# Kernel optimization log

Measured on AMD Instinct MI355X. Metric: run time of the kernel, lower is better.

The kernel has to match this reference:

```python
import jax, jax.numpy as jnp
import numpy as np


def setup_inputs() -> dict:
    key = jax.random.key(0)
    kx, ky = jax.random.split(key)
    x = jax.random.normal(kx, (4, 8192, 3), dtype=jnp.float32)
    y = jax.random.normal(ky, (4, 8192, 3), dtype=jnp.float32)
    return {"x": x, "y": y}


def _chamfer(x, y):
    # x: [B, N, D], y: [B, M, D]
    x2 = jnp.sum(x * x, axis=-1)                      # [B, N]
    y2 = jnp.sum(y * y, axis=-1)                      # [B, M]
    xy = jnp.einsum("bnd,bmd->bnm", x, y)             # [B, N, M]
    d2 = x2[:, :, None] + y2[:, None, :] - 2.0 * xy   # [B, N, M]
    d2 = jnp.maximum(d2, 0.0)
    cham_x = jnp.min(d2, axis=2).mean(axis=1)         # [B] min over M, mean over N
    cham_y = jnp.min(d2, axis=1).mean(axis=1)         # [B] min over N, mean over M
    return cham_x + cham_y                            # [B]


def reference(x, y):
    per_batch = _chamfer(x, y)
    return jnp.mean(per_batch)  # batch_reduction='mean'
```

## Files before the change

### kernel.cpp

```cpp
#include <hip/hip_runtime.h>


#define N_      8192
#define RPB     4096
#define NRECS   16384
#define NQ      65536
#define FLT_BIG 3.0e38f

typedef float v2f  __attribute__((ext_vector_type(2)));
typedef unsigned int v16u __attribute__((ext_vector_type(16)));

__global__ void zero_out_kernel(float* out) { *out = 0.0f; }

__global__ __launch_bounds__(256) void prep_kernel(
    const float* __restrict__ x, const float* __restrict__ y,
    float4* __restrict__ xrec, float4* __restrict__ yrec,
    unsigned int* __restrict__ pmin, float* __restrict__ out)
{
    int i = blockIdx.x * 256 + threadIdx.x;
    if (i == 0) *out = 0.0f;
    pmin[i]         = 0x7F800000u;
    pmin[i + 32768] = 0x7F800000u;
    int side = i >> 14;
    int r    = i & (NRECS - 1);
    const float* src = side ? y : x;
    float4*      dst = side ? yrec : xrec;
    const float* p = src + (size_t)r * 6;
    float p0x = p[0], p0y = p[1], p0z = p[2];
    float p1x = p[3], p1y = p[4], p1z = p[5];
    float w0 = fmaf(p0x, p0x, fmaf(p0y, p0y, p0z * p0z));
    float w1 = fmaf(p1x, p1x, fmaf(p1y, p1y, p1z * p1z));
    dst[2*r]   = make_float4(p0x, p1x, p0y, p1y);
    dst[2*r+1] = make_float4(p0z, p1z, w0, w1);
}


static __device__ __forceinline__ void s_load2(v16u& a, v16u& b, const unsigned int* p) {
    asm volatile("s_load_dwordx16 %0, %2, 0x0\n\t"
                 "s_load_dwordx16 %1, %2, 0x40"
                 : "=s"(a), "=s"(b) : "s"(p));
}
static __device__ __forceinline__ void s_wait(v16u& a, v16u& b) {
    asm volatile("s_waitcnt lgkmcnt(0)" : "+s"(a), "+s"(b));
}

static __device__ __forceinline__ void do_record(
    const unsigned int* d,
    const v2f* qx, const v2f* qy, const v2f* qz,
    float* acc)
{
    v2f pxs = (v2f){__uint_as_float(d[0]), __uint_as_float(d[1])};
    v2f pys = (v2f){__uint_as_float(d[2]), __uint_as_float(d[3])};
    v2f pzs = (v2f){__uint_as_float(d[4]), __uint_as_float(d[5])};
    v2f w2v = (v2f){__uint_as_float(d[6]), __uint_as_float(d[7])};
    #pragma unroll
    for (int j = 0; j < 4; ++j) {
        v2f td, ts;
        asm("v_pk_fma_f32 %0, %1, %2, %3"
            : "=v"(td) : "v"(qz[j]), "s"(pzs), "v"(w2v));
        asm("v_pk_fma_f32 %0, %1, %2, %3 op_sel:[0,1,1] op_sel_hi:[1,0,0]"
            : "=v"(ts) : "v"(qz[j]), "s"(pzs), "v"(w2v));
        asm("v_pk_fma_f32 %0, %1, %2, %0"
            : "+v"(td) : "v"(qy[j]), "s"(pys));
        asm("v_pk_fma_f32 %0, %1, %2, %0 op_sel:[0,1,0] op_sel_hi:[1,0,1]"
            : "+v"(ts) : "v"(qy[j]), "s"(pys));
        asm("v_pk_fma_f32 %0, %1, %2, %0"
            : "+v"(td) : "v"(qx[j]), "s"(pxs));
        asm("v_pk_fma_f32 %0, %1, %2, %0 op_sel:[0,1,0] op_sel_hi:[1,0,1]"
            : "+v"(ts) : "v"(qx[j]), "s"(pxs));
        asm("v_min3_f32 %0, %0, %1, %2" : "+v"(acc[2*j])   : "v"(td.x), "v"(ts.x));
        asm("v_min3_f32 %0, %0, %1, %2" : "+v"(acc[2*j+1]) : "v"(td.y), "v"(ts.y));
    }
}

__global__ __launch_bounds__(512, 4) void chamfer_kernel(
    const float* __restrict__ xraw, const float* __restrict__ yraw,
    const float4* __restrict__ xrec, const float4* __restrict__ yrec,
    unsigned int* __restrict__ pmin)
{
    __shared__ float red[8 * 512];

    const int tid  = threadIdx.x;
    const int lane = tid & 63;
    const int wave = __builtin_amdgcn_readfirstlane(tid >> 6);
    const int blk  = blockIdx.x;
    const int dir   = blk >> 8;
    const int batch = (blk >> 6) & 3;
    const int qg    = (blk >> 2) & 15;
    const int seg   = blk & 3;

    const float*  qraw = dir ? yraw : xraw;
    const float4* orec = dir ? xrec : yrec;

    const int qbase = batch * N_ + qg * 512;
    float f[24];
    {
        const float4* qv = (const float4*)(qraw + (size_t)qbase * 3) + lane * 6;
        #pragma unroll
        for (int k = 0; k < 6; ++k) {
            float4 t = qv[k];
            f[4*k] = t.x; f[4*k+1] = t.y; f[4*k+2] = t.z; f[4*k+3] = t.w;
        }
    }
    v2f qx[4], qy[4], qz[4];
    float acc[8];
    #pragma unroll
    for (int j = 0; j < 4; ++j) {
        qx[j] = (v2f){-2.0f * f[6*j+0], -2.0f * f[6*j+3]};
        qy[j] = (v2f){-2.0f * f[6*j+1], -2.0f * f[6*j+4]};
        qz[j] = (v2f){-2.0f * f[6*j+2], -2.0f * f[6*j+5]};
        acc[2*j] = FLT_BIG; acc[2*j+1] = FLT_BIG;
    }

    const unsigned int* sp = (const unsigned int*)
        (orec + (size_t)2 * (batch * RPB + seg * 1024 + wave * 128));
    v16u a0, a1, b0, b1;
    s_load2(a0, a1, sp);
    for (int g = 0; g < 32; g += 2) {
        s_wait(a0, a1);
        if (g + 1 < 32) s_load2(b0, b1, sp + (g + 1) * 32);
        {
            unsigned int da[16], db[16];
            #pragma unroll
            for (int t = 0; t < 16; ++t) { da[t] = a0[t]; db[t] = a1[t]; }
            do_record(da,     qx, qy, qz, acc);
            do_record(da + 8, qx, qy, qz, acc);
            do_record(db,     qx, qy, qz, acc);
            do_record(db + 8, qx, qy, qz, acc);
        }
        s_wait(b0, b1);
        if (g + 2 < 32) s_load2(a0, a1, sp + (g + 2) * 32);
        {
            unsigned int da[16], db[16];
            #pragma unroll
            for (int t = 0; t < 16; ++t) { da[t] = b0[t]; db[t] = b1[t]; }
            do_record(da,     qx, qy, qz, acc);
            do_record(da + 8, qx, qy, qz, acc);
            do_record(db,     qx, qy, qz, acc);
            do_record(db + 8, qx, qy, qz, acc);
        }
    }

    #pragma unroll
    for (int j = 0; j < 8; ++j) red[wave * 512 + lane * 8 + j] = acc[j];
    __syncthreads();

    float m = red[tid];
    #pragma unroll
    for (int w = 1; w < 8; ++w) m = fminf(m, red[w * 512 + tid]);
    int gq = qbase + tid;
    float ax = qraw[gq*3+0], ay = qraw[gq*3+1], az = qraw[gq*3+2];
    float qn = fmaf(ax, ax, fmaf(ay, ay, az * az));
    float d2 = fmaxf(0.0f, qn + m);
    atomicMin(&pmin[dir * 32768 + gq], __float_as_uint(d2));
}

__global__ __launch_bounds__(256) void sum_kernel(
    const unsigned int* __restrict__ pmin, float* __restrict__ out)
{
    int i = blockIdx.x * 256 + threadIdx.x;
    float4 v = ((const float4*)pmin)[i];
    float s = v.x + v.y + v.z + v.w;
    #pragma unroll
    for (int off = 32; off > 0; off >>= 1) s += __shfl_xor(s, off);
    if ((threadIdx.x & 63) == 0) atomicAdd(out, s * (1.0f / 32768.0f));
}

__global__ __launch_bounds__(1024) void chamfer_raw_kernel(
    const float* __restrict__ xraw, const float* __restrict__ yraw,
    float* __restrict__ out)
{
    __shared__ float4 red4[16][64];
    const int tid  = threadIdx.x;
    const int wave = tid >> 6;
    const int lane = tid & 63;
    const int blk  = blockIdx.x;
    const bool xdir = (blk < 128);
    const int b    = (blk & 127) >> 5;
    const int qofs = (blk & 31) << 8;
    const float* qraw = xdir ? xraw : yraw;
    const float* oraw = xdir ? yraw : xraw;
    float qx0[4], qx1[4], qx2[4], acc[4];
    #pragma unroll
    for (int q = 0; q < 4; ++q) {
        int gq = b * N_ + qofs + lane*4 + q;
        qx0[q] = qraw[gq*3+0]; qx1[q] = qraw[gq*3+1]; qx2[q] = qraw[gq*3+2];
        acc[q] = FLT_BIG;
    }
    const float* opp = oraw + (size_t)(b * N_ + wave * 512) * 3;
    #pragma unroll 4
    for (int k = 0; k < 512; ++k) {
        float p0 = opp[k*3+0], p1 = opp[k*3+1], p2 = opp[k*3+2];
        float w  = fmaf(p0, p0, fmaf(p1, p1, p2*p2));
        #pragma unroll
        for (int q = 0; q < 4; ++q) {
            float dot = qx0[q]*p0 + qx1[q]*p1 + qx2[q]*p2;
            acc[q] = fminf(acc[q], fmaf(-2.0f, dot, w));
        }
    }
    red4[wave][lane] = make_float4(acc[0], acc[1], acc[2], acc[3]);
    __syncthreads();
    if (tid < 256) {
        const float* red = (const float*)red4;
        float m = red[tid];
        #pragma unroll
        for (int w = 1; w < 16; ++w) m = fminf(m, red[w*256 + tid]);
        int gq = b * N_ + qofs + tid;
        float ax = qraw[gq*3+0], ay = qraw[gq*3+1], az = qraw[gq*3+2];
        float d2 = fmaxf(0.0f, fmaf(ax,ax,fmaf(ay,ay,az*az)) + m);
        #pragma unroll
        for (int off = 32; off > 0; off >>= 1) d2 += __shfl_xor(d2, off);
        if ((tid & 63) == 0) atomicAdd(out, d2 * (1.0f / 32768.0f));
    }
}

extern "C" void kernel_launch(void* const* d_in, const int* in_sizes, int n_in,
                              void* d_out, int out_size, void* d_ws, size_t ws_size,
                              hipStream_t stream)
{
    const float* x = (const float*)d_in[0];
    const float* y = (const float*)d_in[1];
    float* out = (float*)d_out;

    const size_t need = (size_t)NRECS * 2 * 2 * sizeof(float4) + NQ * 4;
    if (ws_size >= need) {
        float4* xrec = (float4*)d_ws;
        float4* yrec = xrec + 2 * NRECS;
        unsigned int* pmin = (unsigned int*)(yrec + 2 * NRECS);
        prep_kernel<<<128, 256, 0, stream>>>(x, y, xrec, yrec, pmin, out);
        chamfer_kernel<<<512, 512, 0, stream>>>(x, y, xrec, yrec, pmin);
        sum_kernel<<<64, 256, 0, stream>>>(pmin, out);
    } else {
        zero_out_kernel<<<1, 1, 0, stream>>>(out);
        chamfer_raw_kernel<<<256, 1024, 0, stream>>>(x, y, out);
    }
}
```

Measured before the change: 97.08 us.

## Stage opposite points in LDS per block, double queries per thread

```diff
diff --git a/kernel.cpp b/kernel.cpp
--- a/kernel.cpp
+++ b/kernel.cpp
@@ -2,152 +2,112 @@
 
 
 #define N_      8192
-#define RPB     4096
-#define NRECS   16384
 #define NQ      65536
 #define FLT_BIG 3.0e38f
 
-typedef float v2f  __attribute__((ext_vector_type(2)));
-typedef unsigned int v16u __attribute__((ext_vector_type(16)));
+typedef float v2f __attribute__((ext_vector_type(2)));
 
 __global__ void zero_out_kernel(float* out) { *out = 0.0f; }
 
-__global__ __launch_bounds__(256) void prep_kernel(
-    const float* __restrict__ x, const float* __restrict__ y,
-    float4* __restrict__ xrec, float4* __restrict__ yrec,
-    unsigned int* __restrict__ pmin, float* __restrict__ out)
+__global__ __launch_bounds__(256) void init_kernel(unsigned int* __restrict__ pmin)
 {
     int i = blockIdx.x * 256 + threadIdx.x;
-    if (i == 0) *out = 0.0f;
-    pmin[i]         = 0x7F800000u;
-    pmin[i + 32768] = 0x7F800000u;
-    int side = i >> 14;
-    int r    = i & (NRECS - 1);
-    const float* src = side ? y : x;
-    float4*      dst = side ? yrec : xrec;
-    const float* p = src + (size_t)r * 6;
-    float p0x = p[0], p0y = p[1], p0z = p[2];
-    float p1x = p[3], p1y = p[4], p1z = p[5];
-    float w0 = fmaf(p0x, p0x, fmaf(p0y, p0y, p0z * p0z));
-    float w1 = fmaf(p1x, p1x, fmaf(p1y, p1y, p1z * p1z));
-    dst[2*r]   = make_float4(p0x, p1x, p0y, p1y);
-    dst[2*r+1] = make_float4(p0z, p1z, w0, w1);
-}
-
-
-static __device__ __forceinline__ void s_load2(v16u& a, v16u& b, const unsigned int* p) {
-    asm volatile("s_load_dwordx16 %0, %2, 0x0\n\t"
-                 "s_load_dwordx16 %1, %2, 0x40"
-                 : "=s"(a), "=s"(b) : "s"(p));
-}
-static __device__ __forceinline__ void s_wait(v16u& a, v16u& b) {
-    asm volatile("s_waitcnt lgkmcnt(0)" : "+s"(a), "+s"(b));
-}
-
-static __device__ __forceinline__ void do_record(
-    const unsigned int* d,
-    const v2f* qx, const v2f* qy, const v2f* qz,
-    float* acc)
-{
-    v2f pxs = (v2f){__uint_as_float(d[0]), __uint_as_float(d[1])};
-    v2f pys = (v2f){__uint_as_float(d[2]), __uint_as_float(d[3])};
-    v2f pzs = (v2f){__uint_as_float(d[4]), __uint_as_float(d[5])};
-    v2f w2v = (v2f){__uint_as_float(d[6]), __uint_as_float(d[7])};
-    #pragma unroll
-    for (int j = 0; j < 4; ++j) {
-        v2f td, ts;
-        asm("v_pk_fma_f32 %0, %1, %2, %3"
-            : "=v"(td) : "v"(qz[j]), "s"(pzs), "v"(w2v));
-        asm("v_pk_fma_f32 %0, %1, %2, %3 op_sel:[0,1,1] op_sel_hi:[1,0,0]"
-            : "=v"(ts) : "v"(qz[j]), "s"(pzs), "v"(w2v));
-        asm("v_pk_fma_f32 %0, %1, %2, %0"
-            : "+v"(td) : "v"(qy[j]), "s"(pys));
-        asm("v_pk_fma_f32 %0, %1, %2, %0 op_sel:[0,1,0] op_sel_hi:[1,0,1]"
-            : "+v"(ts) : "v"(qy[j]), "s"(pys));
-        asm("v_pk_fma_f32 %0, %1, %2, %0"
-            : "+v"(td) : "v"(qx[j]), "s"(pxs));
-        asm("v_pk_fma_f32 %0, %1, %2, %0 op_sel:[0,1,0] op_sel_hi:[1,0,1]"
-            : "+v"(ts) : "v"(qx[j]), "s"(pxs));
-        asm("v_min3_f32 %0, %0, %1, %2" : "+v"(acc[2*j])   : "v"(td.x), "v"(ts.x));
-        asm("v_min3_f32 %0, %0, %1, %2" : "+v"(acc[2*j+1]) : "v"(td.y), "v"(ts.y));
-    }
-}
-
-__global__ __launch_bounds__(512, 4) void chamfer_kernel(
+    ((uint4*)pmin)[i] = make_uint4(0x7F800000u, 0x7F800000u, 0x7F800000u, 0x7F800000u);
+}
+
+
+__global__ __launch_bounds__(1024, 4) void chamfer_kernel(
     const float* __restrict__ xraw, const float* __restrict__ yraw,
-    const float4* __restrict__ xrec, const float4* __restrict__ yrec,
     unsigned int* __restrict__ pmin)
 {
-    __shared__ float red[8 * 512];
+    __shared__ float4 lds4[4096];
 
     const int tid  = threadIdx.x;
     const int lane = tid & 63;
     const int wave = __builtin_amdgcn_readfirstlane(tid >> 6);
     const int blk  = blockIdx.x;
-    const int dir   = blk >> 8;
-    const int batch = (blk >> 6) & 3;
-    const int qg    = (blk >> 2) & 15;
+    const int dir   = blk >> 7;
+    const int batch = (blk >> 5) & 3;
+    const int qg    = (blk >> 2) & 7;
     const int seg   = blk & 3;
 
-    const float*  qraw = dir ? yraw : xraw;
-    const float4* orec = dir ? xrec : yrec;
-
-    const int qbase = batch * N_ + qg * 512;
-    float f[24];
+    const float* qraw = dir ? yraw : xraw;
+    const float* oraw = dir ? xraw : yraw;
+
     {
-        const float4* qv = (const float4*)(qraw + (size_t)qbase * 3) + lane * 6;
-        #pragma unroll
-        for (int k = 0; k < 6; ++k) {
+        int r = tid;
+        const float2* p2 = (const float2*)(oraw + ((size_t)batch * N_ + seg * 2048 + 2 * r) * 3);
+        float2 a = p2[0], b = p2[1], c = p2[2];
+        float w0 = fmaf(a.x, a.x, fmaf(a.y, a.y, b.x * b.x));
+        float w1 = fmaf(b.y, b.y, fmaf(c.x, c.x, c.y * c.y));
+        lds4[2*r]   = make_float4(a.x, b.y, a.y, c.x);
+        lds4[2*r+1] = make_float4(b.x, c.y, w0, w1);
+    }
+
+    const int qbase = batch * N_ + qg * 1024;
+    v2f qx[8], qy[8], qz[8];
+    float acc[16];
+    {
+        float f[48];
+        const float4* qv = (const float4*)(qraw + (size_t)qbase * 3) + lane * 12;
+        #pragma unroll
+        for (int k = 0; k < 12; ++k) {
             float4 t = qv[k];
             f[4*k] = t.x; f[4*k+1] = t.y; f[4*k+2] = t.z; f[4*k+3] = t.w;
         }
-    }
-    v2f qx[4], qy[4], qz[4];
-    float acc[8];
-    #pragma unroll
-    for (int j = 0; j < 4; ++j) {
-        qx[j] = (v2f){-2.0f * f[6*j+0], -2.0f * f[6*j+3]};
-        qy[j] = (v2f){-2.0f * f[6*j+1], -2.0f * f[6*j+4]};
-        qz[j] = (v2f){-2.0f * f[6*j+2], -2.0f * f[6*j+5]};
-        acc[2*j] = FLT_BIG; acc[2*j+1] = FLT_BIG;
-    }
-
-    const unsigned int* sp = (const unsigned int*)
-        (orec + (size_t)2 * (batch * RPB + seg * 1024 + wave * 128));
-    v16u a0, a1, b0, b1;
-    s_load2(a0, a1, sp);
-    for (int g = 0; g < 32; g += 2) {
-        s_wait(a0, a1);
-        if (g + 1 < 32) s_load2(b0, b1, sp + (g + 1) * 32);
-        {
-            unsigned int da[16], db[16];
-            #pragma unroll
-            for (int t = 0; t < 16; ++t) { da[t] = a0[t]; db[t] = a1[t]; }
-            do_record(da,     qx, qy, qz, acc);
-            do_record(da + 8, qx, qy, qz, acc);
-            do_record(db,     qx, qy, qz, acc);
-            do_record(db + 8, qx, qy, qz, acc);
-        }
-        s_wait(b0, b1);
-        if (g + 2 < 32) s_load2(a0, a1, sp + (g + 2) * 32);
-        {
-            unsigned int da[16], db[16];
-            #pragma unroll
-            for (int t = 0; t < 16; ++t) { da[t] = b0[t]; db[t] = b1[t]; }
-            do_record(da,     qx, qy, qz, acc);
-            do_record(da + 8, qx, qy, qz, acc);
-            do_record(db,     qx, qy, qz, acc);
-            do_record(db + 8, qx, qy, qz, acc);
-        }
-    }
-
-    #pragma unroll
-    for (int j = 0; j < 8; ++j) red[wave * 512 + lane * 8 + j] = acc[j];
+        #pragma unroll
+        for (int j = 0; j < 8; ++j) {
+            qx[j] = (v2f){-2.0f * f[6*j+0], -2.0f * f[6*j+3]};
+            qy[j] = (v2f){-2.0f * f[6*j+1], -2.0f * f[6*j+4]};
+            qz[j] = (v2f){-2.0f * f[6*j+2], -2.0f * f[6*j+5]};
+            acc[2*j] = FLT_BIG; acc[2*j+1] = FLT_BIG;
+        }
+    }
+    __syncthreads();
+
+    const float4* rp = lds4 + wave * 128;
+    #pragma unroll 8
+    for (int k = 0; k < 64; ++k) {
+        float4 u = rp[2*k];
+        float4 v = rp[2*k+1];
+        v2f px = (v2f){u.x, u.y};
+        v2f py = (v2f){u.z, u.w};
+        v2f pz = (v2f){v.x, v.y};
+        v2f w2 = (v2f){v.z, v.w};
+        #pragma unroll
+        for (int j = 0; j < 8; ++j) {
+            v2f td, ts;
+            asm("v_pk_fma_f32 %0, %1, %2, %3"
+                : "=v"(td) : "v"(qz[j]), "v"(pz), "v"(w2));
+            asm("v_pk_fma_f32 %0, %1, %2, %3 op_sel:[0,1,1] op_sel_hi:[1,0,0]"
+                : "=v"(ts) : "v"(qz[j]), "v"(pz), "v"(w2));
+            asm("v_pk_fma_f32 %0, %1, %2, %0"
+                : "+v"(td) : "v"(qy[j]), "v"(py));
+            asm("v_pk_fma_f32 %0, %1, %2, %0 op_sel:[0,1,0] op_sel_hi:[1,0,1]"
+                : "+v"(ts) : "v"(qy[j]), "v"(py));
+            asm("v_pk_fma_f32 %0, %1, %2, %0"
+                : "+v"(td) : "v"(qx[j]), "v"(px));
+            asm("v_pk_fma_f32 %0, %1, %2, %0 op_sel:[0,1,0] op_sel_hi:[1,0,1]"
+                : "+v"(ts) : "v"(qx[j]), "v"(px));
+            asm("v_min3_f32 %0, %0, %1, %2" : "+v"(acc[2*j])   : "v"(td.x), "v"(ts.x));
+            asm("v_min3_f32 %0, %0, %1, %2" : "+v"(acc[2*j+1]) : "v"(td.y), "v"(ts.y));
+        }
+    }
+    __syncthreads();
+
+    float* red = (float*)lds4;
+    {
+        float4* rw = (float4*)&red[wave * 1024 + lane * 16];
+        rw[0] = make_float4(acc[0],  acc[1],  acc[2],  acc[3]);
+        rw[1] = make_float4(acc[4],  acc[5],  acc[6],  acc[7]);
+        rw[2] = make_float4(acc[8],  acc[9],  acc[10], acc[11]);
+        rw[3] = make_float4(acc[12], acc[13], acc[14], acc[15]);
+    }
     __syncthreads();
 
     float m = red[tid];
     #pragma unroll
-    for (int w = 1; w < 8; ++w) m = fminf(m, red[w * 512 + tid]);
+    for (int w = 1; w < 16; ++w) m = fminf(m, red[w * 1024 + tid]);
     int gq = qbase + tid;
     float ax = qraw[gq*3+0], ay = qraw[gq*3+1], az = qraw[gq*3+2];
     float qn = fmaf(ax, ax, fmaf(ay, ay, az * az));
@@ -155,15 +115,28 @@
     atomicMin(&pmin[dir * 32768 + gq], __float_as_uint(d2));
 }
 
-__global__ __launch_bounds__(256) void sum_kernel(
+__global__ __launch_bounds__(1024) void sum_kernel(
     const unsigned int* __restrict__ pmin, float* __restrict__ out)
 {
-    int i = blockIdx.x * 256 + threadIdx.x;
-    float4 v = ((const float4*)pmin)[i];
-    float s = v.x + v.y + v.z + v.w;
+    __shared__ float sred[16];
+    const int tid = threadIdx.x;
+    const float4* pv = (const float4*)pmin;
+    float s = 0.0f;
+    #pragma unroll
+    for (int k = 0; k < 16; ++k) {
+        float4 v = pv[k * 1024 + tid];
+        s += v.x + v.y + v.z + v.w;
+    }
     #pragma unroll
     for (int off = 32; off > 0; off >>= 1) s += __shfl_xor(s, off);
-    if ((threadIdx.x & 63) == 0) atomicAdd(out, s * (1.0f / 32768.0f));
+    if ((tid & 63) == 0) sred[tid >> 6] = s;
+    __syncthreads();
+    if (tid < 16) {
+        float v = sred[tid];
+        #pragma unroll
+        for (int off = 8; off > 0; off >>= 1) v += __shfl_xor(v, off);
+        if (tid == 0) *out = v * (1.0f / 32768.0f);
+    }
 }
 
 __global__ __launch_bounds__(1024) void chamfer_raw_kernel(
@@ -222,14 +195,12 @@
     const float* y = (const float*)d_in[1];
     float* out = (float*)d_out;
 
-    const size_t need = (size_t)NRECS * 2 * 2 * sizeof(float4) + NQ * 4;
+    const size_t need = (size_t)NQ * 4;
     if (ws_size >= need) {
-        float4* xrec = (float4*)d_ws;
-        float4* yrec = xrec + 2 * NRECS;
-        unsigned int* pmin = (unsigned int*)(yrec + 2 * NRECS);
-        prep_kernel<<<128, 256, 0, stream>>>(x, y, xrec, yrec, pmin, out);
-        chamfer_kernel<<<512, 512, 0, stream>>>(x, y, xrec, yrec, pmin);
-        sum_kernel<<<64, 256, 0, stream>>>(pmin, out);
+        unsigned int* pmin = (unsigned int*)d_ws;
+        init_kernel<<<64, 256, 0, stream>>>(pmin);
+        chamfer_kernel<<<256, 1024, 0, stream>>>(x, y, pmin);
+        sum_kernel<<<1, 1024, 0, stream>>>(pmin, out);
     } else {
         zero_out_kernel<<<1, 1, 0, stream>>>(out);
         chamfer_raw_kernel<<<256, 1024, 0, stream>>>(x, y, out);
```

Result: slower. 99.74 us (+2.7%).
